# Kernel optimization log

Hardware: AMD Instinct MI355X
Metric: run time of the kernel (lower is better)

Reference implementation:

```python
import jax, jax.numpy as jnp
import numpy as np

B, H, W = 4, 128, 128
DIM, HEADS, WS, SS = 192, 6, 16, 8
CAT, NTOK, RD, DTD = 128, 64, 10, 64
MLPH, KSZ = 384, 5
LN_EPS = 1e-5


def _ln(x, g, b):
    mu = jnp.mean(x, axis=-1, keepdims=True)
    var = jnp.mean((x - mu) ** 2, axis=-1, keepdims=True)
    return (x - mu) * jax.lax.rsqrt(var + LN_EPS) * g + b


def _l2n(x):
    n = jnp.sqrt(jnp.sum(x * x, axis=-1, keepdims=True))
    return x / jnp.maximum(n, 1e-12)


def _win_part(x, ws):
    b, h, w, c = x.shape
    x = x.reshape(b, h // ws, ws, w // ws, ws, c).transpose(0, 1, 3, 2, 4, 5)
    return x.reshape(-1, ws, ws, c)


def _win_rev(win, ws, h, w):
    b = win.shape[0] // ((h // ws) * (w // ws))
    x = win.reshape(b, h // ws, w // ws, ws, ws, -1).transpose(0, 1, 3, 2, 4, 5)
    return x.reshape(b, h, w, -1)


def _make_rpi(ws):
    coords = np.stack(np.meshgrid(np.arange(ws), np.arange(ws), indexing='ij'))
    cf = coords.reshape(2, -1)
    rel = (cf[:, :, None] - cf[:, None, :]).transpose(1, 2, 0)
    rel[:, :, 0] += ws - 1
    rel[:, :, 1] += ws - 1
    rel[:, :, 0] *= 2 * ws - 1
    return rel.sum(-1)


def _make_attn_mask(h, w, ws, ss):
    img = np.zeros((1, h, w, 1), np.float32)
    cnt = 0
    for hs in (slice(0, -ws), slice(-ws, -ss), slice(-ss, None)):
        for vs in (slice(0, -ws), slice(-ws, -ss), slice(-ss, None)):
            img[:, hs, vs, :] = cnt
            cnt += 1
    mw = img.reshape(1, h // ws, ws, w // ws, ws, 1).transpose(0, 1, 3, 2, 4, 5).reshape(-1, ws * ws)
    am = mw[:, None, :] - mw[:, :, None]
    return np.where(am != 0, -100.0, 0.0).astype(np.float32)


def _fwd(x, td, attn_mask, rpi, h, w, norm1_g, norm1_b, norm2_g, norm2_b,
         wqkv_w, wqkv_b, wq_w, wq_b, wk_w, wk_b, wv_w, wv_b, atd_scale,
         aca_proj_w, aca_proj_b, rpb_table, win_proj_w, win_proj_b,
         fc_td_w, fc_td_b, fc1_w, fc1_b, dw_w, dw_b, fc2_w, fc2_b):
    b, n, c = x.shape
    shortcut = x
    xn = _ln(x, norm1_g, norm1_b)
    qkv = xn @ wqkv_w + wqkv_b  # (b, n, 3c)

    # --- ATD_CA: normalized cross-attention to token dictionary ---
    q = xn @ wq_w + wq_b          # (b, n, RD)
    k = td @ wk_w + wk_b          # (b, m, RD)
    v = td @ wv_w + wv_b          # (b, m, c)
    sim = jnp.einsum('bnr,bmr->bnm', _l2n(q), _l2n(k))
    scale = 1.0 + jnp.clip(atd_scale, 0.0, 3.0) * np.log(NTOK)
    sim = jax.nn.softmax(sim * scale, axis=-1)
    x_atd = sim @ v               # (b, n, c)

    # --- AC_MSA: category-sorted grouped attention ---
    tk_id = jnp.argmax(sim, axis=-1)                 # (b, n) int
    gs = min(n, CAT)
    ng = (n + gs - 1) // gs
    pad_n = ng * gs - n
    sidx = jnp.argsort(tk_id, axis=-1)
    inv = jnp.argsort(sidx, axis=-1)                 # inverse permutation
    sqkv = jnp.take_along_axis(qkv, sidx[:, :, None], axis=1)
    if pad_n > 0:
        sqkv = jnp.concatenate([sqkv, jnp.flip(sqkv[:, n - pad_n:n, :], axis=1)], axis=1)
    hd = c // HEADS
    g = sqkv.reshape(b, ng, gs, 3, HEADS, hd).transpose(3, 0, 1, 4, 2, 5)
    qg, kg, vg = g[0], g[1], g[2]
    ga = jax.nn.softmax(jnp.einsum('bghqd,bghkd->bghqk', qg, kg) * (hd ** -0.5), axis=-1)
    yg = jnp.einsum('bghqk,bghkd->bghqd', ga, vg).transpose(0, 1, 3, 2, 4).reshape(b, ng * gs, c)[:, :n]
    x_aca = jnp.take_along_axis(yg, inv[:, :, None], axis=1) @ aca_proj_w + aca_proj_b

    # --- per-token gathered token-dict features for the FFN ---
    td_f = td @ fc_td_w + fc_td_b                    # (b, m, DTD)
    x_td = jnp.take_along_axis(td_f, jnp.broadcast_to(tk_id[:, :, None], (b, n, DTD)), axis=1)

    # --- shifted window attention over qkv ---
    qkv_img = qkv.reshape(b, h, w, 3 * c)
    sh = jnp.roll(qkv_img, shift=(-SS, -SS), axis=(1, 2))
    xw = _win_part(sh, WS).reshape(-1, WS * WS, 3 * c)
    b_, nn_ = xw.shape[0], WS * WS
    wq3 = xw.reshape(b_, nn_, 3, HEADS, hd).transpose(2, 0, 3, 1, 4)
    qw, kw, vw = wq3[0] * (hd ** -0.5), wq3[1], wq3[2]
    aw = jnp.einsum('bhqd,bhkd->bhqk', qw, kw)
    rpb = rpb_table[rpi.reshape(-1)].reshape(nn_, nn_, HEADS).transpose(2, 0, 1)
    aw = aw + rpb[None]
    nw = attn_mask.shape[0]
    aw = (aw.reshape(b_ // nw, nw, HEADS, nn_, nn_) + attn_mask[None, :, None]).reshape(b_, HEADS, nn_, nn_)
    aw = jax.nn.softmax(aw, axis=-1)
    yw = jnp.einsum('bhqk,bhkd->bhqd', aw, vw).transpose(0, 2, 1, 3).reshape(b_, nn_, c)
    yw = yw @ win_proj_w + win_proj_b
    yw = _win_rev(yw.reshape(-1, WS, WS, c), WS, h, w)
    x_win = jnp.roll(yw, shift=(SS, SS), axis=(1, 2)).reshape(b, n, c)

    x = shortcut + x_win + x_atd + x_aca

    # --- ConvFFN with concatenated token-dict features + depthwise conv ---
    xn2 = _ln(x, norm2_g, norm2_b)
    x1 = jax.nn.gelu(xn2 @ fc1_w + fc1_b, approximate=False)
    xc = jnp.concatenate([x1, x_td], axis=-1)        # (b, n, MLPH+DTD)
    ch = MLPH + DTD
    img = xc.reshape(b, h, w, ch)
    cv = jax.lax.conv_general_dilated(img, dw_w, (1, 1), 'SAME',
                                      dimension_numbers=('NHWC', 'HWIO', 'NHWC'),
                                      feature_group_count=ch)
    cv = jax.nn.gelu(cv + dw_b, approximate=False).reshape(b, n, ch)
    x = x + (xc + cv) @ fc2_w + fc2_b
    return x


def setup_inputs():
    key = jax.random.key(0)
    ks = jax.random.split(key, 16)
    w02 = lambda k, s: jax.random.normal(k, s, jnp.float32) * 0.02
    return {
        'x': jax.random.normal(ks[0], (B, H * W, DIM), jnp.float32),
        'td': jax.random.normal(ks[1], (B, NTOK, DIM), jnp.float32),
        'attn_mask': jnp.asarray(_make_attn_mask(H, W, WS, SS)),
        'rpi': jnp.asarray(_make_rpi(WS), jnp.int32),
        'h': H, 'w': W,
        'norm1_g': jnp.ones((DIM,)), 'norm1_b': jnp.zeros((DIM,)),
        'norm2_g': jnp.ones((DIM,)), 'norm2_b': jnp.zeros((DIM,)),
        'wqkv_w': w02(ks[2], (DIM, 3 * DIM)), 'wqkv_b': jnp.zeros((3 * DIM,)),
        'wq_w': w02(ks[3], (DIM, RD)), 'wq_b': jnp.zeros((RD,)),
        'wk_w': w02(ks[4], (DIM, RD)), 'wk_b': jnp.zeros((RD,)),
        'wv_w': w02(ks[5], (DIM, DIM)), 'wv_b': jnp.zeros((DIM,)),
        'atd_scale': jnp.ones((1,)),
        'aca_proj_w': w02(ks[6], (DIM, DIM)), 'aca_proj_b': jnp.zeros((DIM,)),
        'rpb_table': w02(ks[7], ((2 * WS - 1) ** 2, HEADS)),
        'win_proj_w': w02(ks[8], (DIM, DIM)), 'win_proj_b': jnp.zeros((DIM,)),
        'fc_td_w': w02(ks[9], (DIM, DTD)), 'fc_td_b': jnp.zeros((DTD,)),
        'fc1_w': w02(ks[10], (DIM, MLPH)), 'fc1_b': jnp.zeros((MLPH,)),
        'dw_w': w02(ks[11], (KSZ, KSZ, 1, MLPH + DTD)), 'dw_b': jnp.zeros((MLPH + DTD,)),
        'fc2_w': w02(ks[12], (MLPH + DTD, DIM)), 'fc2_b': jnp.zeros((DIM,)),
    }


def reference(x, td, attn_mask, rpi, h, w, norm1_g, norm1_b, norm2_g, norm2_b,
              wqkv_w, wqkv_b, wq_w, wq_b, wk_w, wk_b, wv_w, wv_b, atd_scale,
              aca_proj_w, aca_proj_b, rpb_table, win_proj_w, win_proj_b,
              fc_td_w, fc_td_b, fc1_w, fc1_b, dw_w, dw_b, fc2_w, fc2_b):
    return _fwd(x, td, attn_mask, rpi, h, w, norm1_g, norm1_b, norm2_g, norm2_b,
                wqkv_w, wqkv_b, wq_w, wq_b, wk_w, wk_b, wv_w, wv_b, atd_scale,
                aca_proj_w, aca_proj_b, rpb_table, win_proj_w, win_proj_b,
                fc_td_w, fc_td_b, fc1_w, fc1_b, dw_w, dw_b, fc2_w, fc2_b)
```

## Files before the change

### kernel.cpp

```cpp
#include <hip/hip_runtime.h>
#include <hip/hip_bf16.h>
#include <math.h>

typedef __hip_bfloat16 bf16;
typedef short bf16x8 __attribute__((ext_vector_type(8)));
typedef float f32x4 __attribute__((ext_vector_type(4)));

#define NB 4
#define HH 128
#define WWID 128
#define CC 192
#define NPB (HH*WWID)
#define NT (NB*NPB)
#define NHEADS 6
#define HD 32
#define NTOK 64
#define RDIM 10
#define DTD 64
#define MLPH 384
#define CHF (MLPH+DTD)

__device__ __forceinline__ float b2f(bf16 v){ return __bfloat162float(v); }
__device__ __forceinline__ bf16  f2b(float v){ return __float2bfloat16(v); }
__device__ __forceinline__ float bfu(unsigned short u){ return __uint_as_float(((unsigned)u)<<16); }
__device__ __forceinline__ float geluf(float v){ return 0.5f*v*(1.0f+erff(v*0.70710678118654752f)); }
__device__ __forceinline__ int rg3(int v){ return v<112?0:(v<120?1:2); }

__device__ __forceinline__ float wsumf(float v){
  #pragma unroll
  for (int m=32;m>0;m>>=1) v += __shfl_xor(v,m);
  return v;
}

__global__ void k_sentinel(float* out, int n, float v){
  int i = blockIdx.x*256+threadIdx.x;
  if (i<n) out[i]=v;
}

template<int BF16IN>
__global__ __launch_bounds__(256) void k_ln(const float* __restrict__ xf, const bf16* __restrict__ xb,
                                            const float* __restrict__ g, const float* __restrict__ be,
                                            bf16* __restrict__ out){
  int wave = threadIdx.x>>6, lane = threadIdx.x&63;
  int tok = blockIdx.x*4 + wave;
  size_t base = (size_t)tok*CC;
  float v0,v1,v2;
  if (BF16IN){ v0=b2f(xb[base+lane]); v1=b2f(xb[base+lane+64]); v2=b2f(xb[base+lane+128]); }
  else { v0=xf[base+lane]; v1=xf[base+lane+64]; v2=xf[base+lane+128]; }
  float s = wsumf(v0+v1+v2);
  float mu = s*(1.0f/192.0f);
  float d0=v0-mu, d1=v1-mu, d2=v2-mu;
  float q = wsumf(d0*d0+d1*d1+d2*d2);
  float rs = rsqrtf(q*(1.0f/192.0f)+1e-5f);
  out[base+lane]     = f2b(d0*rs*g[lane]     + be[lane]);
  out[base+lane+64]  = f2b(d1*rs*g[lane+64]  + be[lane+64]);
  out[base+lane+128] = f2b(d2*rs*g[lane+128] + be[lane+128]);
}

__global__ __launch_bounds__(256) void k_wt(const float* __restrict__ W, bf16* __restrict__ Wt, int K, int N){
  int i = blockIdx.x*256+threadIdx.x;
  if (i < K*N){ int n = i / K, k = i - n*K; Wt[i] = f2b(W[(size_t)k*N + n]); }
}
__global__ __launch_bounds__(256) void k_cvt(const float* __restrict__ W, bf16* __restrict__ Wb, int n){
  int i = blockIdx.x*256+threadIdx.x;
  if (i < n) Wb[i] = f2b(W[i]);
}

__global__ __launch_bounds__(64) void k_kn(const float* __restrict__ td, const float* __restrict__ wk,
                                           const float* __restrict__ wkb, double* __restrict__ kn){
  int t = blockIdx.x*64+threadIdx.x;
  double kk[10]; double sq=0.0;
  const float* tr = td + (size_t)t*CC;
  #pragma unroll
  for (int r=0;r<10;r++) kk[r]=(double)wkb[r];
  for (int k=0;k<CC;k++){
    double tv=(double)tr[k];
    #pragma unroll
    for (int r=0;r<10;r++) kk[r] += tv*(double)wk[k*10+r];
  }
  #pragma unroll
  for (int r=0;r<10;r++) sq += kk[r]*kk[r];
  double inv = 1.0/fmax(sqrt(sq),1e-12);
  #pragma unroll
  for (int r=0;r<10;r++) kn[t*10+r]=kk[r]*inv;
}

__global__ __launch_bounds__(256) void k_v(const float* __restrict__ td, const float* __restrict__ wv,
                                           const float* __restrict__ wvb, float* __restrict__ vb){
  int idx = blockIdx.x*256+threadIdx.x;
  int c = idx % CC; int bm = idx / CC;
  const float* tr = td + (size_t)bm*CC;
  float a = wvb[c];
  for (int k=0;k<CC;k++) a = fmaf(tr[k], wv[(size_t)k*CC+c], a);
  vb[idx] = a;
}

__global__ __launch_bounds__(256) void k_tdf(const float* __restrict__ td, const float* __restrict__ w,
                                             const float* __restrict__ bb, float* __restrict__ tdf){
  int idx = blockIdx.x*256+threadIdx.x;
  int d = idx & 63; int bm = idx >> 6;
  const float* tr = td + (size_t)bm*CC;
  float a = bb[d];
  for (int k=0;k<CC;k++) a = fmaf(tr[k], w[(size_t)k*64+d], a);
  tdf[idx] = a;
}

__global__ __launch_bounds__(256) void k_rpbq(const int* __restrict__ rpi, const float* __restrict__ rpbt,
                                              bf16* __restrict__ rpbq){
  int idx = blockIdx.x*256+threadIdx.x;
  int h = idx>>16; int qk = idx&65535;
  rpbq[idx] = f2b(rpbt[rpi[qk]*6 + h]);
}

__global__ __launch_bounds__(256) void k_sim(const float* __restrict__ x, const float* __restrict__ n1g,
                                             const float* __restrict__ n1b, const float* __restrict__ wq,
                                             const float* __restrict__ wqb, const double* __restrict__ kn,
                                             const float* __restrict__ atds,
                                             float* __restrict__ sim, int* __restrict__ tkid){
  int wave = threadIdx.x>>6, lane = threadIdx.x&63;
  int tok = blockIdx.x*4 + wave;
  const float* xr = x + (size_t)tok*CC;
  double v0=(double)xr[lane], v1=(double)xr[lane+64], v2=(double)xr[lane+128];
  double s = v0+v1+v2;
  double s2 = v0*v0+v1*v1+v2*v2;
  #pragma unroll
  for (int m=32;m>0;m>>=1){ s += __shfl_xor(s,m); s2 += __shfl_xor(s2,m); }
  double mu = s*(1.0/192.0);
  double var = s2*(1.0/192.0) - mu*mu;
  double rs = 1.0/sqrt(var+1e-5);
  double xn0 = (v0-mu)*rs*(double)n1g[lane]     + (double)n1b[lane];
  double xn1 = (v1-mu)*rs*(double)n1g[lane+64]  + (double)n1b[lane+64];
  double xn2 = (v2-mu)*rs*(double)n1g[lane+128] + (double)n1b[lane+128];
  double q[10]; double sq=0.0;
  #pragma unroll
  for (int r=0;r<10;r++){
    double a = xn0*(double)wq[lane*10+r] + xn1*(double)wq[(lane+64)*10+r] + xn2*(double)wq[(lane+128)*10+r];
    #pragma unroll
    for (int m=32;m>0;m>>=1) a += __shfl_xor(a,m);
    a += (double)wqb[r];
    q[r]=a; sq += a*a;
  }
  double inv = 1.0/fmax(sqrt(sq),1e-12);
  int b = tok>>14;
  const double* kr = kn + ((size_t)((b<<6)+lane))*10;
  double dot=0.0;
  #pragma unroll
  for (int r=0;r<10;r++) dot += q[r]*kr[r];
  dot *= inv;
  double bv=dot; int bi=lane;
  #pragma unroll
  for (int m=32;m>0;m>>=1){
    double ov=__shfl_xor(bv,m); int oi=__shfl_xor(bi,m);
    if (ov>bv || (ov==bv && oi<bi)){ bv=ov; bi=oi; }
  }
  if (lane==0) tkid[tok]=bi;
  double asd = fmin(fmax((double)atds[0],0.0),3.0);
  float t = (float)(dot*(1.0 + asd*4.1588830833596715));
  float mx=t;
  #pragma unroll
  for (int m=32;m>0;m>>=1) mx = fmaxf(mx,__shfl_xor(mx,m));
  float pp = __expf(t-mx);
  float ssf = pp;
  #pragma unroll
  for (int m=32;m>0;m>>=1) ssf += __shfl_xor(ssf,m);
  sim[(size_t)tok*64+lane] = pp/ssf;
}

template<int K, int KC, int NS, int ACT, int OUTMODE>
__global__ __launch_bounds__(256) void k_mm(const bf16* __restrict__ A, const bf16* __restrict__ Wt,
                                            const float* __restrict__ bias, const void* __restrict__ aux,
                                            void* __restrict__ outp){
  __shared__ __align__(16) char As[64*KC*2];
  __shared__ __align__(16) char Ws[64*KC*2];
  int row0 = blockIdx.x*64, n0 = blockIdx.y*64;
  int ti = threadIdx.x;
  int wave = ti>>6, lane = ti&63, g = lane>>4, l15 = lane&15;
  f32x4 acc[4];
  #pragma unroll
  for (int mt=0;mt<4;mt++){ f32x4 z={0.f,0.f,0.f,0.f}; acc[mt]=z; }
  const int KC8 = KC/8;
  for (int c0=0; c0<K; c0+=KC){
    if (c0) __syncthreads();
    for (int u=ti; u<64*KC8; u+=256){
      int r = u/KC8, kc = u-r*KC8;
      uint4 va = *(const uint4*)(A  + (size_t)(row0+r)*K + c0 + kc*8);
      *(uint4*)(As + ((r*(KC*2) + kc*16) ^ ((r&7)<<4))) = va;
      uint4 vw = *(const uint4*)(Wt + (size_t)(n0+r)*K + c0 + kc*8);
      *(uint4*)(Ws + ((r*(KC*2) + kc*16) ^ ((r&7)<<4))) = vw;
    }
    __syncthreads();
    #pragma unroll
    for (int ks=0; ks<KC/32; ks++){
      int rw = wave*16 + l15;
      bf16x8 bfr = *(const bf16x8*)(Ws + ((rw*(KC*2) + ks*64 + g*16) ^ ((rw&7)<<4)));
      #pragma unroll
      for (int mt=0;mt<4;mt++){
        int ra = mt*16 + l15;
        bf16x8 af = *(const bf16x8*)(As + ((ra*(KC*2) + ks*64 + g*16) ^ ((ra&7)<<4)));
        acc[mt] = __builtin_amdgcn_mfma_f32_16x16x32_bf16(af, bfr, acc[mt], 0,0,0);
      }
    }
  }
  int col = n0 + wave*16 + l15;
  float bb = bias[col];
  #pragma unroll
  for (int mt=0;mt<4;mt++){
    #pragma unroll
    for (int j=0;j<4;j++){
      int row = row0 + mt*16 + g*4 + j;
      float v = acc[mt][j] + bb;
      if (OUTMODE==0){
        ((bf16*)outp)[(size_t)row*NS + col] = f2b(ACT ? geluf(v) : v);
      } else if (OUTMODE==2){
        size_t o = (size_t)row*NS + col;
        ((float*)outp)[o] = b2f(((const bf16*)aux)[o]) + v;
      } else if (OUTMODE==3){
        int win=row>>8, tii=row&255;
        int b=win>>6, wloc=win&63;
        int wy=wloc>>3, wx=wloc&7, tyy=tii>>4, txx=tii&15;
        int oy=(wy*16+tyy+8)&127, ox=(wx*16+txx+8)&127;
        size_t o=((size_t)(b*NPB + oy*128 + ox))*NS + col;
        ((bf16*)outp)[o] = f2b(((const float*)aux)[o] + v);
      } else {
        int orow=(row & ~(NPB-1)) + ((const int*)aux)[row];
        size_t o=(size_t)orow*NS + col;
        bf16* xo=(bf16*)outp;
        xo[o] = f2b(b2f(xo[o]) + v);
      }
    }
  }
}

__device__ __forceinline__ float ldw(const bf16* p, size_t i){ return __bfloat162float(p[i]); }
__device__ __forceinline__ float ldw(const float* p, size_t i){ return p[i]; }

template<int KD, int CB, typename WT>
__device__ __forceinline__ void gemm_core(const float (*As)[KD], const WT* __restrict__ W, int N, float (&acc)[8][CB]){
  int tid = threadIdx.x;
  for (int k=0;k<KD;k+=4){
    float w0[CB],w1[CB],w2[CB],w3[CB];
    #pragma unroll
    for (int j=0;j<CB;j++){
      int c = tid + 64*j;
      w0[j]=ldw(W,(size_t)(k+0)*N+c);
      w1[j]=ldw(W,(size_t)(k+1)*N+c);
      w2[j]=ldw(W,(size_t)(k+2)*N+c);
      w3[j]=ldw(W,(size_t)(k+3)*N+c);
    }
    #pragma unroll
    for (int r=0;r<8;r++){
      float4 a = *reinterpret_cast<const float4*>(&As[r][k]);
      #pragma unroll
      for (int j=0;j<CB;j++)
        acc[r][j]=fmaf(a.x,w0[j],fmaf(a.y,w1[j],fmaf(a.z,w2[j],fmaf(a.w,w3[j],acc[r][j]))));
    }
  }
}

__global__ __launch_bounds__(64) void k_xatd(const float* __restrict__ sim, const float* __restrict__ vb,
                                             bf16* __restrict__ xacc){
  __shared__ __align__(16) float As[8][64];
  int row0=blockIdx.x*8;
  for (int idx=threadIdx.x; idx<8*64; idx+=64){
    int r=idx>>6, k=idx&63;
    As[r][k]=sim[(size_t)(row0+r)*64+k];
  }
  __syncthreads();
  float acc[8][3]={};
  const float* Wv = vb + (size_t)(row0>>14)*64*CC;
  gemm_core<64,3>(As, Wv, CC, acc);
  int tid=threadIdx.x;
  #pragma unroll
  for (int j=0;j<3;j++){
    int c=tid+64*j;
    #pragma unroll
    for (int r=0;r<8;r++){
      size_t o=(size_t)(row0+r)*CC+c;
      xacc[o]=f2b(b2f(xacc[o])+acc[r][j]);
    }
  }
}

__global__ __launch_bounds__(256) void k_tdgather(const float* __restrict__ tdf, const int* __restrict__ tkid,
                                                  bf16* __restrict__ xc){
  int idx = blockIdx.x*256+threadIdx.x;
  int d = idx & 63; int tok = idx >> 6;
  int b = tok >> 14;
  int m = tkid[tok];
  xc[(size_t)tok*CHF + MLPH + d] = f2b(tdf[((size_t)((b<<6)+m))*64 + d]);
}

__global__ __launch_bounds__(256) void k_hist(const int* __restrict__ tkid, int* __restrict__ chist){
  __shared__ int h[64];
  int b = blockIdx.x>>6, ch = blockIdx.x&63;
  if (threadIdx.x<64) h[threadIdx.x]=0;
  __syncthreads();
  int v = tkid[b*NPB + ch*256 + threadIdx.x];
  atomicAdd(&h[v],1);
  __syncthreads();
  if (threadIdx.x<64) chist[(size_t)blockIdx.x*64 + threadIdx.x] = h[threadIdx.x];
}

__global__ __launch_bounds__(64) void k_scan(const int* __restrict__ chist, int* __restrict__ coff,
                                             int* __restrict__ bstart){
  int b = blockIdx.x; int v = threadIdx.x;
  __shared__ int tot[64], bs[64];
  int s=0;
  for (int ch=0; ch<64; ch++){
    coff[((size_t)(b*64+ch))*64+v] = s;
    s += chist[((size_t)(b*64+ch))*64+v];
  }
  tot[v]=s;
  __syncthreads();
  if (v==0){ int run=0; for (int u=0;u<64;u++){ bs[u]=run; run+=tot[u]; } }
  __syncthreads();
  bstart[b*64+v] = bs[v];
}

__global__ __launch_bounds__(256) void k_place(const int* __restrict__ tkid, const int* __restrict__ coff,
                                               const int* __restrict__ bstart, int* __restrict__ sidx){
  __shared__ int vals[256];
  int b = blockIdx.x>>6, ch = blockIdx.x&63;
  int tid = threadIdx.x;
  int tok = ch*256 + tid;
  int v = tkid[b*NPB + tok];
  vals[tid]=v;
  __syncthreads();
  int lr=0;
  for (int j=0;j<tid;j++) lr += (vals[j]==v);
  int pos = bstart[b*64+v] + coff[((size_t)(b*64+ch))*64+v] + lr;
  sidx[b*NPB + pos] = tok;
}

__global__ __launch_bounds__(256,4) void k_acattn(const bf16* __restrict__ qkv, const int* __restrict__ sidx,
                                                  bf16* __restrict__ yg){
  __shared__ bf16 Kl[128*32];
  __shared__ bf16 Vt[32*128];
  __shared__ bf16 Ps[4][16*32];
  int bid=blockIdx.x;
  int h = bid % NHEADS; int gg = (bid/NHEADS) & 127; int b = bid/(NHEADS*128);
  int ti = threadIdx.x;
  if (ti < 128){
    int srow = b*NPB + sidx[b*NPB + gg*128 + ti];
    const bf16* src = qkv + (size_t)srow*576 + 192 + h*32;
    const uint4* s4 = (const uint4*)src;
    char* kb = (char*)Kl;
    #pragma unroll
    for (int w=0;w<4;w++) *(uint4*)(kb + ((ti*64 + w*16) ^ ((ti&7)<<4))) = s4[w];
    const bf16* vsrc = src + 192;
    char* vbp = (char*)Vt;
    #pragma unroll
    for (int d=0;d<32;d++) *(bf16*)(vbp + ((d*256 + ti*2) ^ ((d&7)<<4))) = vsrc[d];
  }
  __syncthreads();
  int wave=ti>>6, lane=ti&63, g=lane>>4, l15=lane&15;
  bf16x8 qf[2];
  #pragma unroll
  for (int qt=0;qt<2;qt++){
    int q = wave*32 + qt*16 + l15;
    int srow = b*NPB + sidx[b*NPB + gg*128 + q];
    qf[qt] = *(const bf16x8*)(qkv + (size_t)srow*576 + h*32 + g*8);
  }
  f32x4 O[2][2]; float lsp[2][4];
  #pragma unroll
  for (int qt=0;qt<2;qt++){
    #pragma unroll
    for (int dt=0;dt<2;dt++){ f32x4 z={0.f,0.f,0.f,0.f}; O[qt][dt]=z; }
    #pragma unroll
    for (int j=0;j<4;j++) lsp[qt][j]=0.f;
  }
  const float rsc=0.17677669529663687f;
  const char* kb=(const char*)Kl; const char* vbp=(const char*)Vt;
  for (int st=0; st<4; st++){
    int r0=st*32+l15, r1=st*32+16+l15;
    bf16x8 kf0 = *(const bf16x8*)(kb + ((r0*64 + g*16) ^ ((r0&7)<<4)));
    bf16x8 kf1 = *(const bf16x8*)(kb + ((r1*64 + g*16) ^ ((r1&7)<<4)));
    int d0=l15, d1=16+l15;
    bf16x8 vf0 = *(const bf16x8*)(vbp + ((d0*256 + st*64 + g*16) ^ ((d0&7)<<4)));
    bf16x8 vf1 = *(const bf16x8*)(vbp + ((d1*256 + st*64 + g*16) ^ ((d1&7)<<4)));
    #pragma unroll
    for (int qt=0;qt<2;qt++){
      f32x4 z={0.f,0.f,0.f,0.f};
      f32x4 s0 = __builtin_amdgcn_mfma_f32_16x16x32_bf16(qf[qt], kf0, z, 0,0,0);
      f32x4 s1 = __builtin_amdgcn_mfma_f32_16x16x32_bf16(qf[qt], kf1, z, 0,0,0);
      float p0[4],p1[4];
      char* pb=(char*)Ps[wave];
      #pragma unroll
      for (int j=0;j<4;j++){
        p0[j]=__expf(fminf(s0[j]*rsc,80.f));
        p1[j]=__expf(fminf(s1[j]*rsc,80.f));
        lsp[qt][j]+=p0[j]+p1[j];
        int q=g*4+j;
        *(bf16*)(pb + ((q*64 + l15*2) ^ ((q&7)<<4)))      = f2b(p0[j]);
        *(bf16*)(pb + ((q*64 + 32 + l15*2) ^ ((q&7)<<4))) = f2b(p1[j]);
      }
      bf16x8 pa = *(const bf16x8*)((const char*)Ps[wave] + ((l15*64 + g*16) ^ ((l15&7)<<4)));
      O[qt][0]=__builtin_amdgcn_mfma_f32_16x16x32_bf16(pa, vf0, O[qt][0], 0,0,0);
      O[qt][1]=__builtin_amdgcn_mfma_f32_16x16x32_bf16(pa, vf1, O[qt][1], 0,0,0);
    }
  }
  #pragma unroll
  for (int qt=0;qt<2;qt++){
    #pragma unroll
    for (int msk=1; msk<16; msk<<=1){
      #pragma unroll
      for (int j=0;j<4;j++) lsp[qt][j]+=__shfl_xor(lsp[qt][j],msk);
    }
    #pragma unroll
    for (int j=0;j<4;j++){
      float inv=1.0f/lsp[qt][j];
      int q = wave*32 + qt*16 + g*4 + j;
      bf16* yo = yg + ((size_t)(b*NPB + gg*128 + q))*CC + h*32;
      yo[l15]    = f2b(O[qt][0][j]*inv);
      yo[16+l15] = f2b(O[qt][1][j]*inv);
    }
  }
}

__global__ __launch_bounds__(256,3) void k_winattn(const bf16* __restrict__ qkv, const bf16* __restrict__ rpbq,
                                                   bf16* __restrict__ yw){
  __shared__ bf16 Kl[256*32];
  __shared__ bf16 Vt[32*256];
  __shared__ bf16 Ps[4][16*32];
  int bid = blockIdx.x;
  int h = bid % NHEADS; int win = bid / NHEADS;
  int b = win >> 6; int wloc = win & 63;
  int wy = wloc >> 3, wx = wloc & 7;
  int ti = threadIdx.x;
  {
    int ty=ti>>4, tx=ti&15;
    int oy=(wy*16+ty+8)&127, ox=(wx*16+tx+8)&127;
    const bf16* src = qkv + (size_t)(b*NPB+oy*128+ox)*576 + 192 + h*32;
    const uint4* s4 = (const uint4*)src;
    char* kb = (char*)Kl;
    #pragma unroll
    for (int w=0;w<4;w++) *(uint4*)(kb + ((ti*64 + w*16) ^ ((ti&7)<<4))) = s4[w];
    const bf16* vsrc = src + 192;
    char* vbp = (char*)Vt;
    #pragma unroll
    for (int d=0;d<32;d++) *(bf16*)(vbp + ((d*512 + ti*2) ^ ((d&7)<<4))) = vsrc[d];
  }
  __syncthreads();
  int wave=ti>>6, lane=ti&63, g=lane>>4, l15=lane&15;
  bf16x8 qf[4];
  #pragma unroll
  for (int qt=0;qt<4;qt++){
    int ty=wave*4+qt, tx=l15;
    int oy=(wy*16+ty+8)&127, ox=(wx*16+tx+8)&127;
    qf[qt] = *(const bf16x8*)(qkv + (size_t)(b*NPB+oy*128+ox)*576 + h*32 + g*8);
  }
  f32x4 O[4][2]; float lsp[4][4];
  #pragma unroll
  for (int qt=0;qt<4;qt++){
    #pragma unroll
    for (int dt=0;dt<2;dt++){ f32x4 z={0.f,0.f,0.f,0.f}; O[qt][dt]=z; }
    #pragma unroll
    for (int j=0;j<4;j++) lsp[qt][j]=0.f;
  }
  const float rsc=0.17677669529663687f;
  int rxk = rg3(wx*16+l15);
  int rxq[4], ryq[4];
  #pragma unroll
  for (int j=0;j<4;j++) rxq[j]=rg3(wx*16+g*4+j);
  #pragma unroll
  for (int qt=0;qt<4;qt++) ryq[qt]=rg3(wy*16+wave*4+qt);
  const char* kb=(const char*)Kl; const char* vbp=(const char*)Vt;
  for (int st=0; st<8; st++){
    int r0=st*32+l15, r1=st*32+16+l15;
    bf16x8 kf0 = *(const bf16x8*)(kb + ((r0*64 + g*16) ^ ((r0&7)<<4)));
    bf16x8 kf1 = *(const bf16x8*)(kb + ((r1*64 + g*16) ^ ((r1&7)<<4)));
    int d0=l15, d1=16+l15;
    bf16x8 vf0 = *(const bf16x8*)(vbp + ((d0*512 + st*64 + g*16) ^ ((d0&7)<<4)));
    bf16x8 vf1 = *(const bf16x8*)(vbp + ((d1*512 + st*64 + g*16) ^ ((d1&7)<<4)));
    int rk0 = rg3(wy*16+st*2)*3   + rxk;
    int rk1 = rg3(wy*16+st*2+1)*3 + rxk;
    #pragma unroll
    for (int qt=0;qt<4;qt++){
      f32x4 z={0.f,0.f,0.f,0.f};
      f32x4 s0 = __builtin_amdgcn_mfma_f32_16x16x32_bf16(qf[qt], kf0, z, 0,0,0);
      f32x4 s1 = __builtin_amdgcn_mfma_f32_16x16x32_bf16(qf[qt], kf1, z, 0,0,0);
      int qr0 = wave*64 + qt*16 + g*4;
      float p0[4],p1[4];
      char* pb=(char*)Ps[wave];
      #pragma unroll
      for (int j=0;j<4;j++){
        const bf16* rb = rpbq + (((size_t)h*256 + qr0 + j)<<8) + st*32;
        int rq = ryq[qt]*3 + rxq[j];
        float b0 = b2f(rb[l15])    + (rq!=rk0 ? -100.f : 0.f);
        float b1 = b2f(rb[16+l15]) + (rq!=rk1 ? -100.f : 0.f);
        p0[j]=__expf(fminf(fmaf(s0[j],rsc,b0),80.f));
        p1[j]=__expf(fminf(fmaf(s1[j],rsc,b1),80.f));
        lsp[qt][j]+=p0[j]+p1[j];
        int q=g*4+j;
        *(bf16*)(pb + ((q*64 + l15*2) ^ ((q&7)<<4)))      = f2b(p0[j]);
        *(bf16*)(pb + ((q*64 + 32 + l15*2) ^ ((q&7)<<4))) = f2b(p1[j]);
      }
      bf16x8 pa = *(const bf16x8*)((const char*)Ps[wave] + ((l15*64 + g*16) ^ ((l15&7)<<4)));
      O[qt][0]=__builtin_amdgcn_mfma_f32_16x16x32_bf16(pa, vf0, O[qt][0], 0,0,0);
      O[qt][1]=__builtin_amdgcn_mfma_f32_16x16x32_bf16(pa, vf1, O[qt][1], 0,0,0);
    }
  }
  #pragma unroll
  for (int qt=0;qt<4;qt++){
    #pragma unroll
    for (int msk=1; msk<16; msk<<=1){
      #pragma unroll
      for (int j=0;j<4;j++) lsp[qt][j]+=__shfl_xor(lsp[qt][j],msk);
    }
    #pragma unroll
    for (int j=0;j<4;j++){
      float inv=1.0f/lsp[qt][j];
      int q = wave*64 + qt*16 + g*4 + j;
      bf16* yo = yw + ((size_t)win*256 + q)*CC + h*32;
      yo[l15]    = f2b(O[qt][0][j]*inv);
      yo[16+l15] = f2b(O[qt][1][j]*inv);
    }
  }
}

__global__ __launch_bounds__(256) void k_dw(const bf16* __restrict__ xc, const bf16* __restrict__ dwwb,
                                            const float* __restrict__ dwb, bf16* __restrict__ sv){
  __shared__ uint4 wl[25*56];
  int ti = threadIdx.x;
  for (int i=ti; i<25*56; i+=256) wl[i] = ((const uint4*)dwwb)[i];
  __syncthreads();
  int idx = blockIdx.x*256 + ti;
  int pix = idx/56, ch8 = idx - pix*56;
  int xq = pix&127, yq = (pix>>7)&127, b = pix>>14;
  float acc[8]={0.f,0.f,0.f,0.f,0.f,0.f,0.f,0.f};
  float cen[8];
  #pragma unroll
  for (int dy=0;dy<5;dy++){
    int yy=yq+dy-2;
    if ((unsigned)yy>127u) continue;
    #pragma unroll
    for (int dx=0;dx<5;dx++){
      int xx=xq+dx-2;
      if ((unsigned)xx>127u) continue;
      uint4 v = *(const uint4*)(xc + ((size_t)(b<<14)+(yy<<7)+xx)*CHF + ch8*8);
      uint4 w = wl[(dy*5+dx)*56 + ch8];
      unsigned vv[4]={v.x,v.y,v.z,v.w}, ww[4]={w.x,w.y,w.z,w.w};
      #pragma unroll
      for (int t=0;t<4;t++){
        float i0=bfu((unsigned short)(vv[t]&0xffffu)), i1=bfu((unsigned short)(vv[t]>>16));
        float w0=bfu((unsigned short)(ww[t]&0xffffu)), w1=bfu((unsigned short)(ww[t]>>16));
        acc[2*t]   = fmaf(i0,w0,acc[2*t]);
        acc[2*t+1] = fmaf(i1,w1,acc[2*t+1]);
        if (dy==2 && dx==2){ cen[2*t]=i0; cen[2*t+1]=i1; }
      }
    }
  }
  bf16* o = sv + (size_t)pix*CHF + ch8*8;
  const float* bp = dwb + ch8*8;
  #pragma unroll
  for (int i2=0;i2<8;i2++) o[i2] = f2b(cen[i2] + geluf(acc[i2] + bp[i2]));
}

extern "C" void kernel_launch(void* const* d_in, const int* in_sizes, int n_in,
                              void* d_out, int out_size, void* d_ws, size_t ws_size,
                              hipStream_t stream){
  const float* x    = (const float*)d_in[0];
  const float* td   = (const float*)d_in[1];
  const int*   rpi  = (const int*)d_in[3];
  const float* n1g  = (const float*)d_in[6];
  const float* n1b  = (const float*)d_in[7];
  const float* n2g  = (const float*)d_in[8];
  const float* n2b  = (const float*)d_in[9];
  const float* wqkv = (const float*)d_in[10];
  const float* wqkvb= (const float*)d_in[11];
  const float* wq   = (const float*)d_in[12];
  const float* wqb  = (const float*)d_in[13];
  const float* wk   = (const float*)d_in[14];
  const float* wkb  = (const float*)d_in[15];
  const float* wv   = (const float*)d_in[16];
  const float* wvb  = (const float*)d_in[17];
  const float* atds = (const float*)d_in[18];
  const float* acaw = (const float*)d_in[19];
  const float* acab = (const float*)d_in[20];
  const float* rpbt = (const float*)d_in[21];
  const float* winw = (const float*)d_in[22];
  const float* winb = (const float*)d_in[23];
  const float* tdw  = (const float*)d_in[24];
  const float* tdbb = (const float*)d_in[25];
  const float* f1w  = (const float*)d_in[26];
  const float* f1b  = (const float*)d_in[27];
  const float* dww  = (const float*)d_in[28];
  const float* dwb  = (const float*)d_in[29];
  const float* f2w  = (const float*)d_in[30];
  const float* f2bb = (const float*)d_in[31];
  float* out = (float*)d_out;

  const size_t QKV_BYTES = (size_t)NT*576*2;
  const size_t XN_BYTES  = (size_t)NT*CC*2;
  const size_t XC_BYTES  = (size_t)NT*CHF*2;

  char* base = (char*)d_ws;
  size_t off = 0;
  auto give = [&](size_t bytes)->char*{
    off = (off + 255) & ~(size_t)255;
    char* r = base + off; off += bytes; return r;
  };
  char*   qkv_r = give(QKV_BYTES);
  char*   xn_r  = give(XN_BYTES);
  char*   sim_r = give(XN_BYTES);
  bf16*   xacc  = (bf16*)  give(XN_BYTES);
  int*    tkid  = (int*)   give((size_t)NT*4);
  int*    sidx  = (int*)   give((size_t)NT*4);
  double* kn    = (double*)give((size_t)NB*64*RDIM*8);
  float*  vbuf  = (float*) give((size_t)NB*64*CC*4);
  float*  tdf   = (float*) give((size_t)NB*64*DTD*4);
  int*    chist = (int*)   give((size_t)NB*64*64*4);
  int*    coff  = (int*)   give((size_t)NB*64*64*4);
  int*    bstart= (int*)   give((size_t)NB*64*4);
  bf16*   rpbq  = (bf16*)  give((size_t)NHEADS*256*256*2);
  bf16*   wqkvt = (bf16*)  give((size_t)192*576*2);
  bf16*   f1wt  = (bf16*)  give((size_t)192*384*2);
  bf16*   f2wt  = (bf16*)  give((size_t)448*192*2);
  bf16*   winwt = (bf16*)  give((size_t)192*192*2);
  bf16*   acawt = (bf16*)  give((size_t)192*192*2);
  bf16*   dwwb  = (bf16*)  give((size_t)25*448*2);

  if (off > ws_size){
    k_sentinel<<<(out_size+255)/256,256,0,stream>>>(out, out_size, (float)(ws_size>>20));
    return;
  }

  bf16*  qkv  = (bf16*)qkv_r;
  bf16*  xc   = (bf16*)qkv_r;
  bf16*  sv   = (bf16*)(qkv_r + XC_BYTES);
  bf16*  xn   = (bf16*)xn_r;
  bf16*  atmp = (bf16*)xn_r;
  float* sim  = (float*)sim_r;

  k_wt<<<(192*576+255)/256,256,0,stream>>>(wqkv, wqkvt, 192, 576);
  k_wt<<<(192*384+255)/256,256,0,stream>>>(f1w, f1wt, 192, 384);
  k_wt<<<(448*192+255)/256,256,0,stream>>>(f2w, f2wt, 448, 192);
  k_wt<<<(192*192+255)/256,256,0,stream>>>(winw, winwt, 192, 192);
  k_wt<<<(192*192+255)/256,256,0,stream>>>(acaw, acawt, 192, 192);
  k_cvt<<<(25*448+255)/256,256,0,stream>>>(dww, dwwb, 25*448);
  k_ln<0><<<NT/4,256,0,stream>>>(x, nullptr, n1g, n1b, xn);
  k_mm<192,192,576,0,0><<<dim3(NT/64,9),256,0,stream>>>(xn, wqkvt, wqkvb, nullptr, qkv);
  k_rpbq<<<NHEADS*256*256/256,256,0,stream>>>(rpi, rpbt, rpbq);
  k_winattn<<<NB*64*NHEADS,256,0,stream>>>(qkv, rpbq, atmp);
  k_mm<192,192,192,0,3><<<dim3(NT/64,3),256,0,stream>>>(atmp, winwt, winb, x, xacc);
  k_kn<<<4,64,0,stream>>>(td, wk, wkb, kn);
  k_v<<<(NB*64*CC)/256,256,0,stream>>>(td, wv, wvb, vbuf);
  k_tdf<<<(NB*64*DTD)/256,256,0,stream>>>(td, tdw, tdbb, tdf);
  k_sim<<<NT/4,256,0,stream>>>(x, n1g, n1b, wq, wqb, kn, atds, sim, tkid);
  k_hist<<<NB*64,256,0,stream>>>(tkid, chist);
  k_scan<<<NB,64,0,stream>>>(chist, coff, bstart);
  k_place<<<NB*64,256,0,stream>>>(tkid, coff, bstart, sidx);
  k_acattn<<<NB*128*NHEADS,256,0,stream>>>(qkv, sidx, atmp);
  k_mm<192,192,192,0,4><<<dim3(NT/64,3),256,0,stream>>>(atmp, acawt, acab, sidx, xacc);
  k_xatd<<<NT/8,64,0,stream>>>(sim, vbuf, xacc);
  k_tdgather<<<NT*64/256,256,0,stream>>>(tdf, tkid, xc);
  k_ln<1><<<NT/4,256,0,stream>>>(nullptr, xacc, n2g, n2b, xn);
  k_mm<192,192,448,1,0><<<dim3(NT/64,6),256,0,stream>>>(xn, f1wt, f1b, nullptr, xc);
  k_dw<<<NT*56/256,256,0,stream>>>(xc, dwwb, dwb, sv);
  k_mm<448,224,192,0,2><<<dim3(NT/64,3),256,0,stream>>>(sv, f2wt, f2bb, xacc, out);
}
```

Baseline: 668.2 us.

## Register-block depthwise conv over four pixels per thread with fp32 weights

The depthwise 5x5 conv kernel now has each thread compute four horizontally adjacent output pixels for eight channels. Each input row segment is loaded once and reused across the overlapping taps, which cuts global loads per output from 25 to about 10 per row. Weights are read directly as fp32 from the input instead of going through a separate bf16 conversion kernel and shared memory, so one launch and one sync go away. In exchange each thread uses more registers and there are four times fewer threads.

```diff
diff --git a/kernel.cpp b/kernel.cpp
--- a/kernel.cpp
+++ b/kernel.cpp
@@ -60,10 +60,6 @@
 __global__ __launch_bounds__(256) void k_wt(const float* __restrict__ W, bf16* __restrict__ Wt, int K, int N){
   int i = blockIdx.x*256+threadIdx.x;
   if (i < K*N){ int n = i / K, k = i - n*K; Wt[i] = f2b(W[(size_t)k*N + n]); }
-}
-__global__ __launch_bounds__(256) void k_cvt(const float* __restrict__ W, bf16* __restrict__ Wb, int n){
-  int i = blockIdx.x*256+threadIdx.x;
-  if (i < n) Wb[i] = f2b(W[i]);
 }
 
 __global__ __launch_bounds__(64) void k_kn(const float* __restrict__ td, const float* __restrict__ wk,
@@ -518,42 +514,74 @@
   }
 }
 
-__global__ __launch_bounds__(256) void k_dw(const bf16* __restrict__ xc, const bf16* __restrict__ dwwb,
-                                            const float* __restrict__ dwb, bf16* __restrict__ sv){
-  __shared__ uint4 wl[25*56];
-  int ti = threadIdx.x;
-  for (int i=ti; i<25*56; i+=256) wl[i] = ((const uint4*)dwwb)[i];
-  __syncthreads();
-  int idx = blockIdx.x*256 + ti;
-  int pix = idx/56, ch8 = idx - pix*56;
-  int xq = pix&127, yq = (pix>>7)&127, b = pix>>14;
-  float acc[8]={0.f,0.f,0.f,0.f,0.f,0.f,0.f,0.f};
-  float cen[8];
+__global__ __launch_bounds__(256,4) void k_dw(const bf16* __restrict__ xc, const float* __restrict__ dww,
+                                              const float* __restrict__ dwb, bf16* __restrict__ sv){
+  int tid = blockIdx.x*256 + threadIdx.x;
+  int ch8 = tid % 56; int pt = tid / 56;
+  int x0 = (pt & 31)*4; int yq = (pt>>5)&127; int b = pt>>12;
+  float acc[4][8];
+  #pragma unroll
+  for (int p=0;p<4;p++)
+    #pragma unroll
+    for (int c=0;c<8;c++) acc[p][c]=0.f;
+  unsigned choff = (unsigned)ch8*8;
+  const float* wp = dww + choff;
   #pragma unroll
   for (int dy=0;dy<5;dy++){
-    int yy=yq+dy-2;
+    int yy = yq+dy-2;
     if ((unsigned)yy>127u) continue;
+    float4 w0[5], w1[5];
     #pragma unroll
     for (int dx=0;dx<5;dx++){
-      int xx=xq+dx-2;
-      if ((unsigned)xx>127u) continue;
-      uint4 v = *(const uint4*)(xc + ((size_t)(b<<14)+(yy<<7)+xx)*CHF + ch8*8);
-      uint4 w = wl[(dy*5+dx)*56 + ch8];
-      unsigned vv[4]={v.x,v.y,v.z,v.w}, ww[4]={w.x,w.y,w.z,w.w};
+      w0[dx] = *(const float4*)(wp + (dy*5+dx)*CHF);
+      w1[dx] = *(const float4*)(wp + (dy*5+dx)*CHF + 4);
+    }
+    unsigned rowoff = ((unsigned)(b<<14) + ((unsigned)yy<<7))*CHF + choff;
+    #pragma unroll
+    for (int j=0;j<8;j++){
+      int ox = x0-2+j;
+      if ((unsigned)ox>127u) continue;
+      uint4 v = *(const uint4*)(xc + rowoff + (unsigned)ox*CHF);
+      float u[8];
+      unsigned vv[4]={v.x,v.y,v.z,v.w};
       #pragma unroll
       for (int t=0;t<4;t++){
-        float i0=bfu((unsigned short)(vv[t]&0xffffu)), i1=bfu((unsigned short)(vv[t]>>16));
-        float w0=bfu((unsigned short)(ww[t]&0xffffu)), w1=bfu((unsigned short)(ww[t]>>16));
-        acc[2*t]   = fmaf(i0,w0,acc[2*t]);
-        acc[2*t+1] = fmaf(i1,w1,acc[2*t+1]);
-        if (dy==2 && dx==2){ cen[2*t]=i0; cen[2*t+1]=i1; }
+        u[2*t]  = __uint_as_float(vv[t]<<16);
+        u[2*t+1]= __uint_as_float(vv[t]&0xffff0000u);
       }
-    }
-  }
-  bf16* o = sv + (size_t)pix*CHF + ch8*8;
-  const float* bp = dwb + ch8*8;
-  #pragma unroll
-  for (int i2=0;i2<8;i2++) o[i2] = f2b(cen[i2] + geluf(acc[i2] + bp[i2]));
+      #pragma unroll
+      for (int dx=0;dx<5;dx++){
+        int p = j-dx;
+        if (p<0 || p>3) continue;
+        acc[p][0]=fmaf(u[0],w0[dx].x,acc[p][0]);
+        acc[p][1]=fmaf(u[1],w0[dx].y,acc[p][1]);
+        acc[p][2]=fmaf(u[2],w0[dx].z,acc[p][2]);
+        acc[p][3]=fmaf(u[3],w0[dx].w,acc[p][3]);
+        acc[p][4]=fmaf(u[4],w1[dx].x,acc[p][4]);
+        acc[p][5]=fmaf(u[5],w1[dx].y,acc[p][5]);
+        acc[p][6]=fmaf(u[6],w1[dx].z,acc[p][6]);
+        acc[p][7]=fmaf(u[7],w1[dx].w,acc[p][7]);
+      }
+    }
+  }
+  float4 b0 = *(const float4*)(dwb + choff);
+  float4 b1 = *(const float4*)(dwb + choff + 4);
+  float bb[8]={b0.x,b0.y,b0.z,b0.w,b1.x,b1.y,b1.z,b1.w};
+  unsigned obase = ((unsigned)(b<<14) + ((unsigned)yq<<7) + (unsigned)x0)*CHF + choff;
+  #pragma unroll
+  for (int p=0;p<4;p++){
+    uint4 cv4 = *(const uint4*)(xc + obase + (unsigned)p*CHF);
+    unsigned vv[4]={cv4.x,cv4.y,cv4.z,cv4.w};
+    bf16 o[8];
+    #pragma unroll
+    for (int t=0;t<4;t++){
+      float c0 = __uint_as_float(vv[t]<<16);
+      float c1 = __uint_as_float(vv[t]&0xffff0000u);
+      o[2*t]   = f2b(c0 + geluf(acc[p][2*t]  + bb[2*t]));
+      o[2*t+1] = f2b(c1 + geluf(acc[p][2*t+1]+ bb[2*t+1]));
+    }
+    *(uint4*)(sv + obase + (unsigned)p*CHF) = *(const uint4*)o;
+  }
 }
 
 extern "C" void kernel_launch(void* const* d_in, const int* in_sizes, int n_in,
@@ -618,7 +646,6 @@
   bf16*   f2wt  = (bf16*)  give((size_t)448*192*2);
   bf16*   winwt = (bf16*)  give((size_t)192*192*2);
   bf16*   acawt = (bf16*)  give((size_t)192*192*2);
-  bf16*   dwwb  = (bf16*)  give((size_t)25*448*2);
 
   if (off > ws_size){
     k_sentinel<<<(out_size+255)/256,256,0,stream>>>(out, out_size, (float)(ws_size>>20));
@@ -637,7 +664,6 @@
   k_wt<<<(448*192+255)/256,256,0,stream>>>(f2w, f2wt, 448, 192);
   k_wt<<<(192*192+255)/256,256,0,stream>>>(winw, winwt, 192, 192);
   k_wt<<<(192*192+255)/256,256,0,stream>>>(acaw, acawt, 192, 192);
-  k_cvt<<<(25*448+255)/256,256,0,stream>>>(dww, dwwb, 25*448);
   k_ln<0><<<NT/4,256,0,stream>>>(x, nullptr, n1g, n1b, xn);
   k_mm<192,192,576,0,0><<<dim3(NT/64,9),256,0,stream>>>(xn, wqkvt, wqkvb, nullptr, qkv);
   k_rpbq<<<NHEADS*256*256/256,256,0,stream>>>(rpi, rpbt, rpbq);
@@ -656,6 +682,6 @@
   k_tdgather<<<NT*64/256,256,0,stream>>>(tdf, tkid, xc);
   k_ln<1><<<NT/4,256,0,stream>>>(nullptr, xacc, n2g, n2b, xn);
   k_mm<192,192,448,1,0><<<dim3(NT/64,6),256,0,stream>>>(xn, f1wt, f1b, nullptr, xc);
-  k_dw<<<NT*56/256,256,0,stream>>>(xc, dwwb, dwb, sv);
+  k_dw<<<NT*56/4/256,256,0,stream>>>(xc, dww, dwb, sv);
   k_mm<448,224,192,0,2><<<dim3(NT/64,3),256,0,stream>>>(sv, f2wt, f2bb, xacc, out);
 }
```

Result: faster. 611.6 us (-8.5%).
